# Performance work log

Measured on AMD Instinct MI355X. Metric: run time of the kernel, lower is better.

## Reference

```python
import jax, jax.numpy as jnp
import numpy as np

INT8_MAX = 127.0
EQN = 'bsd,df->bsf'


def _quantize(x, axes):
    """Symmetric int8 abs-max quantization over contraction axes.

    Returns (q, scale) with q in [-127, 127] (stored fp32) and scale shaped
    with keepdims so that q * scale ~ x.
    """
    absmax = jnp.max(jnp.abs(x), axis=axes, keepdims=True)
    scale = absmax / INT8_MAX
    scale = jnp.where(scale == 0.0, jnp.ones_like(scale), scale)
    q = jnp.clip(jnp.round(x / scale), -INT8_MAX, INT8_MAX)
    return q, scale


def setup_inputs() -> dict:
    key = jax.random.key(0)
    k1, k2 = jax.random.split(key)
    lhs = jax.random.normal(k1, (4, 2048, 4096), dtype=jnp.float32)
    rhs = jax.random.normal(k2, (4096, 16384), dtype=jnp.float32)
    return {"lhs": lhs, "rhs": rhs}


def reference(lhs, rhs):
    # AQT quantized einsum 'bsd,df->bsf':
    #   per-(b,s)-row int8 quantization of lhs over contraction axis d,
    #   per-column (f) int8 quantization of rhs over contraction axis d,
    #   low-precision matmul, then dequantize by the outer product of scales.
    q_lhs, s_lhs = _quantize(lhs, axes=(2,))   # q:[b,s,d], s:[b,s,1]
    q_rhs, s_rhs = _quantize(rhs, axes=(0,))   # q:[d,f],  s:[1,f]
    acc = jnp.einsum(EQN, q_lhs, q_rhs)        # int-valued accumulation in fp32
    # dequant: scales factor out of the contraction
    return acc * s_lhs * s_rhs[None]           # [b,s,f]
```

## Files before the change

kernel.cpp:

```cpp
#include <hip/hip_runtime.h>
#include <hip/hip_bf16.h>
#include <stdint.h>

#define M_TOT 8192
#define N_TOT 16384
#define K_TOT 4096

typedef int v4i __attribute__((ext_vector_type(4)));

__device__ __forceinline__ float fix_scale(float s) { return s == 0.0f ? 1.0f : s; }

__device__ __forceinline__ void gload_lds16(const void* g, void* l) {
    __builtin_amdgcn_global_load_lds((__attribute__((address_space(1))) void*)g,
                                     (__attribute__((address_space(3))) void*)l,
                                     16, 0, 0);
}

__device__ __forceinline__ int swz(int byte_off) {
    return byte_off ^ (((byte_off >> 7) & 3) << 4);
}

__device__ __forceinline__ int8_t quant1(float x, float scale) {
    float r = fminf(127.0f, fmaxf(-127.0f, rintf(x / scale)));
    return (int8_t)(int)r;
}

__global__ __launch_bounds__(256) void k_quant_lhs(const float* __restrict__ x,
                                                   int8_t* __restrict__ q,
                                                   float* __restrict__ s) {
    const int row = blockIdx.x;
    const int t = threadIdx.x;
    const float* xr = x + (size_t)row * K_TOT;
    float4 v[4];
    float m = 0.0f;
#pragma unroll
    for (int i = 0; i < 4; ++i) {
        v[i] = ((const float4*)xr)[i * 256 + t];
        m = fmaxf(m, fmaxf(fmaxf(fabsf(v[i].x), fabsf(v[i].y)),
                           fmaxf(fabsf(v[i].z), fabsf(v[i].w))));
    }
#pragma unroll
    for (int off = 32; off; off >>= 1) m = fmaxf(m, __shfl_xor(m, off));
    __shared__ float wmax[4];
    if ((t & 63) == 0) wmax[t >> 6] = m;
    __syncthreads();
    m = fmaxf(fmaxf(wmax[0], wmax[1]), fmaxf(wmax[2], wmax[3]));
    const float scale = fix_scale(m / 127.0f);
    if (t == 0) s[row] = scale;
    unsigned* qrow = (unsigned*)(q + (size_t)row * K_TOT);
#pragma unroll
    for (int i = 0; i < 4; ++i) {
        unsigned b0 = (unsigned char)quant1(v[i].x, scale);
        unsigned b1 = (unsigned char)quant1(v[i].y, scale);
        unsigned b2 = (unsigned char)quant1(v[i].z, scale);
        unsigned b3 = (unsigned char)quant1(v[i].w, scale);
        qrow[i * 256 + t] = b0 | (b1 << 8) | (b2 << 16) | (b3 << 24);
    }
}

__global__ __launch_bounds__(256) void k_rhs_absmax(const float* __restrict__ rhs,
                                                    unsigned* __restrict__ amax) {
    const int f = blockIdx.x * 256 + threadIdx.x;
    const int d0 = blockIdx.y * 256;
    const float* p = rhs + (size_t)d0 * N_TOT + f;
    float m = 0.0f;
#pragma unroll 4
    for (int d = 0; d < 256; ++d)
        m = fmaxf(m, fabsf(p[(size_t)d * N_TOT]));
    atomicMax(amax + f, __float_as_uint(m));
}

__global__ __launch_bounds__(256) void k_rhs_scale(const unsigned* __restrict__ amax,
                                                   float* __restrict__ s) {
    const int f = blockIdx.x * 256 + threadIdx.x;
    s[f] = fix_scale(__uint_as_float(amax[f]) / 127.0f);
}

__global__ __launch_bounds__(256) void k_quant_rhs_t(const float* __restrict__ rhs,
                                                     const float* __restrict__ s,
                                                     int8_t* __restrict__ qT) {
    const int f0 = blockIdx.x * 64;
    const int d0 = blockIdx.y * 64;
    const int t = threadIdx.x;
    __shared__ float sc[64];
    __shared__ alignas(16) int8_t tile[64][64];
    if (t < 64) sc[t] = s[f0 + t];
    __syncthreads();
    const int fl = (t & 15) * 4;
    const int rl = t >> 4;
#pragma unroll
    for (int i = 0; i < 4; ++i) {
        const int dl = i * 16 + rl;
        float4 v = *(const float4*)(rhs + (size_t)(d0 + dl) * N_TOT + f0 + fl);
        tile[fl + 0][dl] = quant1(v.x, sc[fl + 0]);
        tile[fl + 1][dl] = quant1(v.y, sc[fl + 1]);
        tile[fl + 2][dl] = quant1(v.z, sc[fl + 2]);
        tile[fl + 3][dl] = quant1(v.w, sc[fl + 3]);
    }
    __syncthreads();
    const int fr = t >> 2;
    const int dc = (t & 3) * 16;
    *(int4*)(qT + (size_t)(f0 + fr) * K_TOT + d0 + dc) = *(const int4*)&tile[fr][dc];
}

#define BM 256
#define BN 128
#define BK 64
#define NKT (K_TOT / BK)

__global__ __launch_bounds__(512, 4) void k_gemm(const int8_t* __restrict__ qA,
                                                 const int8_t* __restrict__ qB,
                                                 const float* __restrict__ sA,
                                                 const float* __restrict__ sB,
                                                 float* __restrict__ C) {
    __shared__ alignas(1024) int8_t As[3][BM * BK];
    __shared__ alignas(1024) int8_t Bs[3][BN * BK];

    const int bid = blockIdx.x;
    const int sc = bid >> 7;
    const int ii = bid & 127;
    const int bm0 = (ii & 31) << 8;
    const int bn0 = (((sc << 2) | (ii >> 5))) << 7;

    const int tid = threadIdx.x;
    const int wave = tid >> 6;
    const int lane = tid & 63;
    const int wm = (wave >> 1) * 64;
    const int wn = (wave & 1) * 64;

    const int8_t* aSrc[2];
    const int8_t* bSrc;
    {
#pragma unroll
        for (int i = 0; i < 2; ++i) {
            const int l = swz(i * 8192 + tid * 16);
            aSrc[i] = qA + (size_t)(bm0 + (l >> 6)) * K_TOT + (l & 63);
        }
        const int l = swz(tid * 16);
        bSrc = qB + (size_t)(bn0 + (l >> 6)) * K_TOT + (l & 63);
    }

    int offA[4], offB[4];
#pragma unroll
    for (int f = 0; f < 4; ++f) {
        offA[f] = swz((wm + f * 16 + (lane & 15)) * BK + (lane >> 4) * 16);
        offB[f] = swz((wn + f * 16 + (lane & 15)) * BK + (lane >> 4) * 16);
    }

    v4i acc[4][4];
#pragma unroll
    for (int i = 0; i < 4; ++i)
#pragma unroll
        for (int j = 0; j < 4; ++j) {
            v4i z = {0, 0, 0, 0};
            acc[i][j] = z;
        }

    auto stage = [&](int kt, int b) {
#pragma unroll
        for (int i = 0; i < 2; ++i)
            gload_lds16(aSrc[i] + kt * BK, &As[b][i * 8192 + tid * 16]);
        gload_lds16(bSrc + kt * BK, &Bs[b][tid * 16]);
    };

    stage(0, 0);
    stage(1, 1);
    asm volatile("s_waitcnt vmcnt(3)" ::: "memory");
    __builtin_amdgcn_s_barrier();

    int bufc = 0;
    for (int kt = 0; kt < NKT; ++kt) {
        const int bnext = (bufc == 2) ? 0 : bufc + 1;
        const int bstage = (bnext == 2) ? 0 : bnext + 1;
        if (kt + 2 < NKT) stage(kt + 2, bstage);

        const int8_t* a = As[bufc];
        const int8_t* b = Bs[bufc];
        v4i af[4], bf[4];
#pragma unroll
        for (int f = 0; f < 4; ++f) {
            af[f] = *(const v4i*)(a + offA[f]);
            bf[f] = *(const v4i*)(b + offB[f]);
        }

        __builtin_amdgcn_s_setprio(1);
#pragma unroll
        for (int f = 0; f < 4; ++f)
#pragma unroll
            for (int j = 0; j < 4; ++j)
                acc[f][j] = __builtin_amdgcn_mfma_i32_16x16x64_i8(af[f], bf[j], acc[f][j], 0, 0, 0);
        __builtin_amdgcn_s_setprio(0);

        if (kt + 1 < NKT) {
            if (kt + 2 < NKT) asm volatile("s_waitcnt vmcnt(3)" ::: "memory");
            else              asm volatile("s_waitcnt vmcnt(0)" ::: "memory");
            __builtin_amdgcn_s_barrier();
        }
        bufc = bnext;
    }

    const int cc = lane & 15;
    const int cr = (lane >> 4) * 4;
#pragma unroll
    for (int mi = 0; mi < 4; ++mi) {
        const int gr0 = bm0 + wm + mi * 16 + cr;
        float sa[4];
#pragma unroll
        for (int r = 0; r < 4; ++r) sa[r] = sA[gr0 + r];
#pragma unroll
        for (int j = 0; j < 4; ++j) {
            const int gc = bn0 + wn + j * 16 + cc;
            const float sb = sB[gc];
#pragma unroll
            for (int r = 0; r < 4; ++r)
                C[(size_t)(gr0 + r) * N_TOT + gc] = (float)acc[mi][j][r] * sa[r] * sb;
        }
    }
}

extern "C" void kernel_launch(void* const* d_in, const int* in_sizes, int n_in,
                              void* d_out, int out_size, void* d_ws, size_t ws_size,
                              hipStream_t stream) {
    const float* lhs = (const float*)d_in[0];
    const float* rhs = (const float*)d_in[1];
    float* out = (float*)d_out;
    char* ws = (char*)d_ws;

    int8_t* qA = (int8_t*)ws;
    int8_t* qB = (int8_t*)(ws + (size_t)33554432);
    float* sA = (float*)(ws + (size_t)33554432 + 67108864);
    float* sB = sA + M_TOT;
    unsigned* amax = (unsigned*)(sB + N_TOT);

    hipMemsetAsync(amax, 0, N_TOT * sizeof(unsigned), stream);

    k_quant_lhs<<<M_TOT, 256, 0, stream>>>(lhs, qA, sA);
    k_rhs_absmax<<<dim3(N_TOT / 256, K_TOT / 256), 256, 0, stream>>>(rhs, amax);
    k_rhs_scale<<<N_TOT / 256, 256, 0, stream>>>(amax, sB);
    k_quant_rhs_t<<<dim3(N_TOT / 64, K_TOT / 64), 256, 0, stream>>>(rhs, sB, qB);
    k_gemm<<<(M_TOT / BM) * (N_TOT / BN), 512, 0, stream>>>(qA, qB, sA, sB, out);
}
```

Baseline: 818.4 us.

## Switch GEMM to 32x32x32 int8 MFMA with 4 waves and larger per-wave tiles

The int8 GEMM now uses 256 threads (4 waves) per block instead of 512. Each wave computes a 128x64 sub-tile with 32x32x32 i8 MFMA instructions in place of 16x16x64, which raises per-wave operand reuse and cuts the number of LDS fragment reads per MFMA. The global-to-LDS staging is spread over more loads per thread, and the wait counts and epilogue indexing are adjusted to the 32x32 accumulator layout. In exchange, each thread holds more accumulator registers, fewer waves are resident, and there may be less latency hiding.

Result: slower. 903.4 us (+10.4%).

```diff
diff --git a/kernel.cpp b/kernel.cpp
--- a/kernel.cpp
+++ b/kernel.cpp
@@ -7,6 +7,7 @@
 #define K_TOT 4096
 
 typedef int v4i __attribute__((ext_vector_type(4)));
+typedef int v16i __attribute__((ext_vector_type(16)));
 
 __device__ __forceinline__ float fix_scale(float s) { return s == 0.0f ? 1.0f : s; }
 
@@ -108,7 +109,7 @@
 #define BK 64
 #define NKT (K_TOT / BK)
 
-__global__ __launch_bounds__(512, 4) void k_gemm(const int8_t* __restrict__ qA,
+__global__ __launch_bounds__(256, 2) void k_gemm(const int8_t* __restrict__ qA,
                                                  const int8_t* __restrict__ qB,
                                                  const float* __restrict__ sA,
                                                  const float* __restrict__ sB,
@@ -120,100 +121,113 @@
     const int sc = bid >> 7;
     const int ii = bid & 127;
     const int bm0 = (ii & 31) << 8;
-    const int bn0 = (((sc << 2) | (ii >> 5))) << 7;
+    const int bn0 = ((sc << 2) | (ii >> 5)) << 7;
 
     const int tid = threadIdx.x;
     const int wave = tid >> 6;
     const int lane = tid & 63;
-    const int wm = (wave >> 1) * 64;
+    const int wm = (wave >> 1) * 128;
     const int wn = (wave & 1) * 64;
 
-    const int8_t* aSrc[2];
-    const int8_t* bSrc;
-    {
-#pragma unroll
-        for (int i = 0; i < 2; ++i) {
-            const int l = swz(i * 8192 + tid * 16);
-            aSrc[i] = qA + (size_t)(bm0 + (l >> 6)) * K_TOT + (l & 63);
-        }
-        const int l = swz(tid * 16);
-        bSrc = qB + (size_t)(bn0 + (l >> 6)) * K_TOT + (l & 63);
-    }
-
-    int offA[4], offB[4];
+    const int8_t* aSrc[4];
+    const int8_t* bSrc[2];
+#pragma unroll
+    for (int i = 0; i < 4; ++i) {
+        const int l = swz(i * 4096 + tid * 16);
+        aSrc[i] = qA + (size_t)(bm0 + (l >> 6)) * K_TOT + (l & 63);
+    }
+#pragma unroll
+    for (int i = 0; i < 2; ++i) {
+        const int l = swz(i * 4096 + tid * 16);
+        bSrc[i] = qB + (size_t)(bn0 + (l >> 6)) * K_TOT + (l & 63);
+    }
+
+    int offA0[4], offA1[4], offB0[2], offB1[2];
 #pragma unroll
     for (int f = 0; f < 4; ++f) {
-        offA[f] = swz((wm + f * 16 + (lane & 15)) * BK + (lane >> 4) * 16);
-        offB[f] = swz((wn + f * 16 + (lane & 15)) * BK + (lane >> 4) * 16);
-    }
-
-    v4i acc[4][4];
-#pragma unroll
-    for (int i = 0; i < 4; ++i)
-#pragma unroll
-        for (int j = 0; j < 4; ++j) {
-            v4i z = {0, 0, 0, 0};
-            acc[i][j] = z;
-        }
-
-    auto stage = [&](int kt, int b) {
+        const int base = (wm + f * 32 + (lane & 31)) * BK + (lane >> 5) * 16;
+        offA0[f] = swz(base);
+        offA1[f] = swz(base + 32);
+    }
+#pragma unroll
+    for (int n = 0; n < 2; ++n) {
+        const int base = (wn + n * 32 + (lane & 31)) * BK + (lane >> 5) * 16;
+        offB0[n] = swz(base);
+        offB1[n] = swz(base + 32);
+    }
+
+    v16i acc[4][2];
+#pragma unroll
+    for (int f = 0; f < 4; ++f)
+#pragma unroll
+        for (int n = 0; n < 2; ++n)
+#pragma unroll
+            for (int e = 0; e < 16; ++e) acc[f][n][e] = 0;
+
+    auto stage = [&](int kt) {
+        const int b = kt % 3;
+#pragma unroll
+        for (int i = 0; i < 4; ++i)
+            gload_lds16(aSrc[i] + kt * BK, &As[b][i * 4096 + tid * 16]);
 #pragma unroll
         for (int i = 0; i < 2; ++i)
-            gload_lds16(aSrc[i] + kt * BK, &As[b][i * 8192 + tid * 16]);
-        gload_lds16(bSrc + kt * BK, &Bs[b][tid * 16]);
+            gload_lds16(bSrc[i] + kt * BK, &Bs[b][i * 4096 + tid * 16]);
     };
 
-    stage(0, 0);
-    stage(1, 1);
-    asm volatile("s_waitcnt vmcnt(3)" ::: "memory");
+    stage(0);
+    stage(1);
+    asm volatile("s_waitcnt vmcnt(6)" ::: "memory");
     __builtin_amdgcn_s_barrier();
 
-    int bufc = 0;
     for (int kt = 0; kt < NKT; ++kt) {
-        const int bnext = (bufc == 2) ? 0 : bufc + 1;
-        const int bstage = (bnext == 2) ? 0 : bnext + 1;
-        if (kt + 2 < NKT) stage(kt + 2, bstage);
-
-        const int8_t* a = As[bufc];
-        const int8_t* b = Bs[bufc];
-        v4i af[4], bf[4];
+        if (kt + 2 < NKT) stage(kt + 2);
+
+        const int8_t* a = As[kt % 3];
+        const int8_t* b = Bs[kt % 3];
+        v4i af0[4], af1[4], bf0[2], bf1[2];
 #pragma unroll
         for (int f = 0; f < 4; ++f) {
-            af[f] = *(const v4i*)(a + offA[f]);
-            bf[f] = *(const v4i*)(b + offB[f]);
+            af0[f] = *(const v4i*)(a + offA0[f]);
+            af1[f] = *(const v4i*)(a + offA1[f]);
+        }
+#pragma unroll
+        for (int n = 0; n < 2; ++n) {
+            bf0[n] = *(const v4i*)(b + offB0[n]);
+            bf1[n] = *(const v4i*)(b + offB1[n]);
         }
 
         __builtin_amdgcn_s_setprio(1);
 #pragma unroll
         for (int f = 0; f < 4; ++f)
 #pragma unroll
-            for (int j = 0; j < 4; ++j)
-                acc[f][j] = __builtin_amdgcn_mfma_i32_16x16x64_i8(af[f], bf[j], acc[f][j], 0, 0, 0);
+            for (int n = 0; n < 2; ++n)
+                acc[f][n] = __builtin_amdgcn_mfma_i32_32x32x32_i8(af0[f], bf0[n], acc[f][n], 0, 0, 0);
+#pragma unroll
+        for (int f = 0; f < 4; ++f)
+#pragma unroll
+            for (int n = 0; n < 2; ++n)
+                acc[f][n] = __builtin_amdgcn_mfma_i32_32x32x32_i8(af1[f], bf1[n], acc[f][n], 0, 0, 0);
         __builtin_amdgcn_s_setprio(0);
 
         if (kt + 1 < NKT) {
-            if (kt + 2 < NKT) asm volatile("s_waitcnt vmcnt(3)" ::: "memory");
+            if (kt + 2 < NKT) asm volatile("s_waitcnt vmcnt(6)" ::: "memory");
             else              asm volatile("s_waitcnt vmcnt(0)" ::: "memory");
             __builtin_amdgcn_s_barrier();
         }
-        bufc = bnext;
-    }
-
-    const int cc = lane & 15;
-    const int cr = (lane >> 4) * 4;
-#pragma unroll
-    for (int mi = 0; mi < 4; ++mi) {
-        const int gr0 = bm0 + wm + mi * 16 + cr;
-        float sa[4];
-#pragma unroll
-        for (int r = 0; r < 4; ++r) sa[r] = sA[gr0 + r];
-#pragma unroll
-        for (int j = 0; j < 4; ++j) {
-            const int gc = bn0 + wn + j * 16 + cc;
-            const float sb = sB[gc];
-#pragma unroll
-            for (int r = 0; r < 4; ++r)
-                C[(size_t)(gr0 + r) * N_TOT + gc] = (float)acc[mi][j][r] * sa[r] * sb;
+    }
+
+    const int cc0 = lane & 31;
+    const int rbase = (lane >> 5) * 4;
+#pragma unroll
+    for (int f = 0; f < 4; ++f) {
+#pragma unroll
+        for (int r = 0; r < 16; ++r) {
+            const int gr = bm0 + wm + f * 32 + (r & 3) + 8 * (r >> 2) + rbase;
+            const float sa = sA[gr];
+            float* crow = C + (size_t)gr * N_TOT + bn0 + wn;
+#pragma unroll
+            for (int n = 0; n < 2; ++n)
+                crow[n * 32 + cc0] = (float)acc[f][n][r] * sa * sB[bn0 + wn + n * 32 + cc0];
         }
     }
 }
@@ -238,5 +252,5 @@
     k_rhs_absmax<<<dim3(N_TOT / 256, K_TOT / 256), 256, 0, stream>>>(rhs, amax);
     k_rhs_scale<<<N_TOT / 256, 256, 0, stream>>>(amax, sB);
     k_quant_rhs_t<<<dim3(N_TOT / 64, K_TOT / 64), 256, 0, stream>>>(rhs, sB, qB);
-    k_gemm<<<(M_TOT / BM) * (N_TOT / BN), 512, 0, stream>>>(qA, qB, sA, sB, out);
-}
+    k_gemm<<<(M_TOT / BM) * (N_TOT / BN), 256, 0, stream>>>(qA, qB, sA, sB, out);
+}
```
